# Kernel optimization log

Measured on AMD Instinct MI355X. Metric: run time of the kernel, lower is better.

## Reference

```python
import jax, jax.numpy as jnp
import numpy as np

N_NODES = 40000
N_EDGES = 640000
D_IN = 128
D_HID = 128
D_OUT = 128
N_GRAPHS = 128


def setup_inputs() -> dict:
    key = jax.random.key(0)
    ks = jax.random.split(key, 12)
    x = jax.random.normal(ks[0], (N_NODES, D_IN), dtype=jnp.float32)
    edge_index = jax.random.randint(ks[1], (2, N_EDGES), 0, N_NODES, dtype=jnp.int64)
    batch = jnp.sort(jax.random.randint(ks[2], (N_NODES,), 0, N_GRAPHS, dtype=jnp.int64))
    def lin(k, fan_in, shape):
        s = 1.0 / np.sqrt(fan_in)
        return jax.random.uniform(k, shape, dtype=jnp.float32, minval=-s, maxval=s)
    return {
        "x": x, "edge_index": edge_index, "batch": batch,
        "W_rel0": lin(ks[3], D_IN, (D_IN, D_HID)), "b_rel0": lin(ks[4], D_IN, (D_HID,)), "W_root0": lin(ks[5], D_IN, (D_IN, D_HID)),
        "W_rel1": lin(ks[6], D_HID, (D_HID, D_HID)), "b_rel1": lin(ks[7], D_HID, (D_HID,)), "W_root1": lin(ks[8], D_HID, (D_HID, D_HID)),
        "W_rel2": lin(ks[9], D_HID, (D_HID, D_OUT)), "b_rel2": lin(ks[10], D_HID, (D_OUT,)), "W_root2": lin(ks[11], D_HID, (D_HID, D_OUT)),
    }


def graph_conv(x, src, dst, W_rel, b_rel, W_root):
    # PyG GraphConv: out_i = Lin_rel(sum_{j in N(i)} x_j) + Lin_root(x_i)
    agg = jax.ops.segment_sum(x[src], dst, num_segments=N_NODES)  # [N, F]
    return agg @ W_rel + b_rel + x @ W_root


def reference(x, edge_index, batch,
              W_rel0, b_rel0, W_root0,
              W_rel1, b_rel1, W_root1,
              W_rel2, b_rel2, W_root2):
    src, dst = edge_index[0], edge_index[1]
    h = graph_conv(x, src, dst, W_rel0, b_rel0, W_root0)
    h = jax.nn.relu(h)  # dropout is identity in eval mode
    h = graph_conv(h, src, dst, W_rel1, b_rel1, W_root1)
    h = jax.nn.relu(h)
    h = graph_conv(h, src, dst, W_rel2, b_rel2, W_root2)
    # global_max_pool over per-node graph ids -> [n_graphs, D_OUT]
    return jax.ops.segment_max(h, batch, num_segments=N_GRAPHS)
```

## Files before the change

### kernel.cpp

```cpp
#include <hip/hip_runtime.h>
#include <hip/hip_bf16.h>
#include <math.h>

#define N_NODES 40000
#define N_EDGES 640000
#define D 128
#define N_GRAPHS 128
#define SCAN_NBLK ((N_NODES + 255) / 256)
#define LDS_STRIDE 68

typedef __attribute__((ext_vector_type(8))) short bf16x8;
typedef __attribute__((ext_vector_type(4))) float f32x4;
typedef __attribute__((ext_vector_type(4))) unsigned int u32x4;

static __device__ __forceinline__ unsigned short f2b(float f) {
    unsigned int u = __float_as_uint(f);
    unsigned int r = (u + 0x7fffu + ((u >> 16) & 1u)) >> 16;
    return (unsigned short)r;
}
static __device__ __forceinline__ float blo(unsigned int u) {
    return __uint_as_float(u << 16);
}
static __device__ __forceinline__ float bhi(unsigned int u) {
    return __uint_as_float(u & 0xffff0000u);
}

__global__ void k_hist(const int* __restrict__ ei, int* __restrict__ counts) {
    int e = blockIdx.x * blockDim.x + threadIdx.x;
    if (e < N_EDGES) atomicAdd(&counts[ei[N_EDGES + e]], 1);
}

__global__ void __launch_bounds__(256) k_scan1(const int* __restrict__ counts,
                                               int* __restrict__ local_pre,
                                               int* __restrict__ blocksums) {
    int t = threadIdx.x;
    int i = blockIdx.x * 256 + t;
    int lane = t & 63, wave = t >> 6;
    int v = (i < N_NODES) ? ((counts[i] + 7) & ~7) : 0;
    int incl = v;
#pragma unroll
    for (int off = 1; off < 64; off <<= 1) {
        int u = __shfl_up(incl, off);
        if (lane >= off) incl += u;
    }
    __shared__ int ws[4];
    if (lane == 63) ws[wave] = incl;
    __syncthreads();
    int base = 0;
    for (int w = 0; w < 4; ++w) {
        int s = ws[w];
        if (w < wave) base += s;
    }
    if (i < N_NODES) local_pre[i] = base + incl - v;
    if (t == 255) blocksums[blockIdx.x] = base + incl;
}

__global__ void __launch_bounds__(256) k_scan2(int* __restrict__ blocksums) {
    int t = threadIdx.x;
    int lane = t & 63, wave = t >> 6;
    int v = (t < SCAN_NBLK) ? blocksums[t] : 0;
    int incl = v;
#pragma unroll
    for (int off = 1; off < 64; off <<= 1) {
        int u = __shfl_up(incl, off);
        if (lane >= off) incl += u;
    }
    __shared__ int ws[4];
    if (lane == 63) ws[wave] = incl;
    __syncthreads();
    int base = 0;
    for (int w = 0; w < 4; ++w) {
        int s = ws[w];
        if (w < wave) base += s;
    }
    if (t < SCAN_NBLK) blocksums[t] = base + incl - v;
}

__global__ void __launch_bounds__(256) k_scan3(const int* __restrict__ local_pre,
                                               const int* __restrict__ blocksums,
                                               const int* __restrict__ counts,
                                               int* __restrict__ rp_pad,
                                               int* __restrict__ cursor) {
    int i = blockIdx.x * 256 + threadIdx.x;
    if (i < N_NODES) {
        int rp = blocksums[blockIdx.x] + local_pre[i];
        rp_pad[i] = rp;
        cursor[i] = rp;
        if (i == N_NODES - 1) rp_pad[N_NODES] = rp + ((counts[i] + 7) & ~7);
    }
}

__global__ void k_scatter(const int* __restrict__ ei, int* __restrict__ cursor,
                          int* __restrict__ src_pad) {
    int e = blockIdx.x * blockDim.x + threadIdx.x;
    if (e < N_EDGES) {
        int d = ei[N_EDGES + e];
        int pos = atomicAdd(&cursor[d], 1);
        src_pad[pos] = ei[e];
    }
}

__global__ void k_pad(const int* __restrict__ cursor, const int* __restrict__ rp_pad,
                      int* __restrict__ src_pad) {
    int i = blockIdx.x * blockDim.x + threadIdx.x;
    if (i >= N_NODES) return;
    int s = cursor[i], e = rp_pad[i + 1];
    for (int j = s; j < e; ++j) src_pad[j] = N_NODES;
}

__global__ void k_bounds(const int* __restrict__ batch, int* __restrict__ bounds) {
    int n = blockIdx.x * blockDim.x + threadIdx.x;
    if (n >= N_NODES) return;
    int b = batch[n];
    if (n == 0) {
        for (int g = 0; g <= b; ++g) bounds[g] = 0;
    } else {
        int pb = batch[n - 1];
        for (int g = pb + 1; g <= b; ++g) bounds[g] = n;
    }
    if (n == N_NODES - 1) {
        for (int g = b + 1; g <= N_GRAPHS; ++g) bounds[g] = N_NODES;
    }
}

__global__ void k_x2b(const float* __restrict__ x, unsigned int* __restrict__ xb) {
    int i = blockIdx.x * blockDim.x + threadIdx.x;
    if (i >= N_NODES * D / 8) return;
    const f32x4* xv = (const f32x4*)x;
    f32x4 v0 = xv[i * 2], v1 = xv[i * 2 + 1];
    u32x4 o;
    o.x = ((unsigned int)f2b(v0.y) << 16) | f2b(v0.x);
    o.y = ((unsigned int)f2b(v0.w) << 16) | f2b(v0.z);
    o.z = ((unsigned int)f2b(v1.y) << 16) | f2b(v1.x);
    o.w = ((unsigned int)f2b(v1.w) << 16) | f2b(v1.z);
    ((u32x4*)xb)[i] = o;
}

__global__ void k_wprep3(const float* __restrict__ Wr0, const float* __restrict__ Wt0,
                         const float* __restrict__ Wr1, const float* __restrict__ Wt1,
                         const float* __restrict__ Wr2, const float* __restrict__ Wt2,
                         unsigned short* __restrict__ WT) {
    int l = blockIdx.x >> 7, c = blockIdx.x & 127, k = threadIdx.x;
    const float* Wrel = (l == 0) ? Wr0 : (l == 1) ? Wr1 : Wr2;
    const float* Wroot = (l == 0) ? Wt0 : (l == 1) ? Wt1 : Wt2;
    float v = (k < D) ? Wrel[k * D + c] : Wroot[(k - D) * D + c];
    WT[(size_t)l * 128 * 256 + c * 256 + k] = f2b(v);
}

__global__ void __launch_bounds__(256) k_layer(
    const unsigned short* __restrict__ in,
    const int* __restrict__ rp_pad,
    const int* __restrict__ src_pad,
    const unsigned short* __restrict__ WT,
    const float* __restrict__ bias,
    unsigned short* __restrict__ out,
    int relu) {
    __shared__ unsigned int aggLDS[16 * LDS_STRIDE];
    int tid = threadIdx.x;
    int w = tid >> 6;
    int lane = tid & 63;
    int q = lane >> 4;
    int c = lane & 15;
    int nl = w * 4 + q;
    int nodebase = blockIdx.x * 16;
    const u32x4* inv = (const u32x4*)in;

    int s = rp_pad[nodebase + nl];
    int e = rp_pad[nodebase + nl + 1];
    const int4* sidx = (const int4*)(src_pad + s);
    int ntrips = (e - s) >> 3;

    float a0 = 0.f, a1 = 0.f, a2 = 0.f, a3 = 0.f;
    float a4 = 0.f, a5 = 0.f, a6 = 0.f, a7 = 0.f;

#define ACC8(v) do { \
        a0 += blo((v).x); a1 += bhi((v).x); \
        a2 += blo((v).y); a3 += bhi((v).y); \
        a4 += blo((v).z); a5 += bhi((v).z); \
        a6 += blo((v).w); a7 += bhi((v).w); } while (0)

    for (int t = 0; t < ntrips; ++t) {
        int4 ia = sidx[2 * t];
        int4 ib = sidx[2 * t + 1];
        u32x4 v0 = inv[ia.x * 16 + c];
        u32x4 v1 = inv[ia.y * 16 + c];
        u32x4 v2 = inv[ia.z * 16 + c];
        u32x4 v3 = inv[ia.w * 16 + c];
        u32x4 v4 = inv[ib.x * 16 + c];
        u32x4 v5 = inv[ib.y * 16 + c];
        u32x4 v6 = inv[ib.z * 16 + c];
        u32x4 v7 = inv[ib.w * 16 + c];
        ACC8(v0); ACC8(v1); ACC8(v2); ACC8(v3);
        ACC8(v4); ACC8(v5); ACC8(v6); ACC8(v7);
    }
#undef ACC8

    u32x4 o;
    o.x = ((unsigned int)f2b(a1) << 16) | f2b(a0);
    o.y = ((unsigned int)f2b(a3) << 16) | f2b(a2);
    o.z = ((unsigned int)f2b(a5) << 16) | f2b(a4);
    o.w = ((unsigned int)f2b(a7) << 16) | f2b(a6);
    *(u32x4*)&aggLDS[nl * LDS_STRIDE + c * 4] = o;
    __syncthreads();

    int row = c, quad = q;
    int colbase = w * 32;

    f32x4 acc0 = {0.f, 0.f, 0.f, 0.f};
    f32x4 acc1 = {0.f, 0.f, 0.f, 0.f};

    const unsigned int* Al = &aggLDS[row * LDS_STRIDE];
    const short* Xp = (const short*)(in + (nodebase + row) * D);
    const short* W0 = (const short*)(WT + (colbase + row) * 256);
    const short* W1 = (const short*)(WT + (colbase + 16 + row) * 256);

#pragma unroll
    for (int t = 0; t < 4; ++t) {
        bf16x8 af = *(const bf16x8*)(Al + t * 16 + quad * 4);
        int k0 = t * 32 + quad * 8;
        bf16x8 b0 = *(const bf16x8*)(W0 + k0);
        bf16x8 b1 = *(const bf16x8*)(W1 + k0);
        acc0 = __builtin_amdgcn_mfma_f32_16x16x32_bf16(af, b0, acc0, 0, 0, 0);
        acc1 = __builtin_amdgcn_mfma_f32_16x16x32_bf16(af, b1, acc1, 0, 0, 0);
    }
#pragma unroll
    for (int t = 0; t < 4; ++t) {
        int k0 = t * 32 + quad * 8;
        bf16x8 xf = *(const bf16x8*)(Xp + k0);
        bf16x8 b0 = *(const bf16x8*)(W0 + 128 + k0);
        bf16x8 b1 = *(const bf16x8*)(W1 + 128 + k0);
        acc0 = __builtin_amdgcn_mfma_f32_16x16x32_bf16(xf, b0, acc0, 0, 0, 0);
        acc1 = __builtin_amdgcn_mfma_f32_16x16x32_bf16(xf, b1, acc1, 0, 0, 0);
    }

    int c0 = colbase + row, c1 = c0 + 16;
    float bia0 = bias[c0], bia1 = bias[c1];
#pragma unroll
    for (int r = 0; r < 4; ++r) {
        int n2 = nodebase + quad * 4 + r;
        float v0 = acc0[r] + bia0;
        float v1 = acc1[r] + bia1;
        if (relu) { v0 = fmaxf(v0, 0.f); v1 = fmaxf(v1, 0.f); }
        out[n2 * D + c0] = f2b(v0);
        out[n2 * D + c1] = f2b(v1);
    }
}

__global__ void __launch_bounds__(512) k_segmax(const unsigned short* __restrict__ h,
                                                const int* __restrict__ bounds,
                                                float* __restrict__ out) {
    __shared__ float sm[8][128];
    int g = blockIdx.x;
    int tid = threadIdx.x;
    int rg = tid >> 6;
    int c = tid & 63;
    int s = bounds[g], e = bounds[g + 1];
    const unsigned int* h32 = (const unsigned int*)h;

    float m0 = -INFINITY, m1 = -INFINITY;
    int n = s + rg;
    for (; n + 8 < e; n += 16) {
        unsigned int v0 = h32[n * 64 + c];
        unsigned int v1 = h32[(n + 8) * 64 + c];
        m0 = fmaxf(m0, blo(v0)); m1 = fmaxf(m1, bhi(v0));
        m0 = fmaxf(m0, blo(v1)); m1 = fmaxf(m1, bhi(v1));
    }
    if (n < e) {
        unsigned int v0 = h32[n * 64 + c];
        m0 = fmaxf(m0, blo(v0)); m1 = fmaxf(m1, bhi(v0));
    }
    sm[rg][c * 2] = m0;
    sm[rg][c * 2 + 1] = m1;
    __syncthreads();
    if (tid < 128) {
        float m = sm[0][tid];
#pragma unroll
        for (int r = 1; r < 8; ++r) m = fmaxf(m, sm[r][tid]);
        out[g * D + tid] = m;
    }
}

extern "C" void kernel_launch(void* const* d_in, const int* in_sizes, int n_in,
                              void* d_out, int out_size, void* d_ws, size_t ws_size,
                              hipStream_t stream) {
    const float* x = (const float*)d_in[0];
    const int* ei = (const int*)d_in[1];
    const int* batch = (const int*)d_in[2];
    const float* Wrel[3]  = {(const float*)d_in[3], (const float*)d_in[6], (const float*)d_in[9]};
    const float* brel[3]  = {(const float*)d_in[4], (const float*)d_in[7], (const float*)d_in[10]};
    const float* Wroot[3] = {(const float*)d_in[5], (const float*)d_in[8], (const float*)d_in[11]};
    float* out = (float*)d_out;

    char* ws = (char*)d_ws;
    size_t off = 0;
    auto alloc = [&](size_t bytes) -> void* {
        void* p = ws + off;
        off = (off + bytes + 255) & ~(size_t)255;
        return p;
    };
    unsigned short* xb  = (unsigned short*)alloc((size_t)(N_NODES + 1) * D * 2);
    unsigned short* hA  = (unsigned short*)alloc((size_t)(N_NODES + 1) * D * 2);
    unsigned short* hB  = (unsigned short*)alloc((size_t)(N_NODES + 1) * D * 2);
    unsigned short* WT  = (unsigned short*)alloc((size_t)3 * 128 * 256 * 2);
    int* rp_pad     = (int*)alloc((size_t)(N_NODES + 1) * 4);
    int* counts     = (int*)alloc((size_t)N_NODES * 4);
    int* cursor     = (int*)alloc((size_t)N_NODES * 4);
    int* src_pad    = (int*)alloc((size_t)(N_EDGES + 8 * N_NODES) * 4);
    int* bounds     = (int*)alloc((size_t)(N_GRAPHS + 1) * 4);
    int* local_pre  = (int*)alloc((size_t)N_NODES * 4);
    int* blocksums  = (int*)alloc((size_t)SCAN_NBLK * 4);

    hipMemsetAsync(counts, 0, (size_t)N_NODES * 4, stream);
    hipMemsetAsync(xb + (size_t)N_NODES * D, 0, D * 2, stream);
    hipMemsetAsync(hA + (size_t)N_NODES * D, 0, D * 2, stream);
    hipMemsetAsync(hB + (size_t)N_NODES * D, 0, D * 2, stream);

    k_hist<<<(N_EDGES + 255) / 256, 256, 0, stream>>>(ei, counts);
    k_scan1<<<SCAN_NBLK, 256, 0, stream>>>(counts, local_pre, blocksums);
    k_scan2<<<1, 256, 0, stream>>>(blocksums);
    k_scan3<<<SCAN_NBLK, 256, 0, stream>>>(local_pre, blocksums, counts, rp_pad, cursor);
    k_scatter<<<(N_EDGES + 255) / 256, 256, 0, stream>>>(ei, cursor, src_pad);
    k_pad<<<SCAN_NBLK, 256, 0, stream>>>(cursor, rp_pad, src_pad);
    k_bounds<<<(N_NODES + 255) / 256, 256, 0, stream>>>(batch, bounds);

    k_x2b<<<(N_NODES * D / 8 + 255) / 256, 256, 0, stream>>>(x, (unsigned int*)xb);
    k_wprep3<<<384, 256, 0, stream>>>(Wrel[0], Wroot[0], Wrel[1], Wroot[1],
                                      Wrel[2], Wroot[2], WT);

    const unsigned short* in = xb;
    unsigned short* houts[3] = {hA, hB, hA};
    for (int l = 0; l < 3; ++l) {
        k_layer<<<N_NODES / 16, 256, 0, stream>>>(in, rp_pad, src_pad,
                                                  WT + (size_t)l * 128 * 256,
                                                  brel[l], houts[l], (l < 2) ? 1 : 0);
        in = houts[l];
    }

    k_segmax<<<N_GRAPHS, 512, 0, stream>>>(houts[2], bounds, out);
}
```

Measured before the change: 295.6 us.

## Fuse preprocessing kernels and pad neighbor lists to multiples of sixteen

Four memsets and several small preprocessing kernels (histogram, bounds, x-to-bf16 conversion, weight packing, padding) are merged into two launches, k_init and k_pack1, and padding is moved into the scan step. Each node's neighbor list is now padded to a multiple of 16 instead of 8, so the aggregation loop issues 16 independent gathers per iteration. The aim is to cut launch overhead and raise memory-level parallelism in the gather. In exchange, padding gathers of the zero row grow, since each node now averages about 16 edges against a padded length of up to 31.

```diff
diff --git a/kernel.cpp b/kernel.cpp
--- a/kernel.cpp
+++ b/kernel.cpp
@@ -25,9 +25,66 @@
     return __uint_as_float(u & 0xffff0000u);
 }
 
-__global__ void k_hist(const int* __restrict__ ei, int* __restrict__ counts) {
-    int e = blockIdx.x * blockDim.x + threadIdx.x;
-    if (e < N_EDGES) atomicAdd(&counts[ei[N_EDGES + e]], 1);
+__global__ void __launch_bounds__(256) k_init(
+    const int* __restrict__ batch, int* __restrict__ counts,
+    int* __restrict__ bounds,
+    unsigned short* __restrict__ xb, unsigned short* __restrict__ hA,
+    unsigned short* __restrict__ hB) {
+    int n = blockIdx.x * 256 + threadIdx.x;
+    if (n < N_NODES) {
+        counts[n] = 0;
+        int b = batch[n];
+        if (n == 0) {
+            for (int g = 0; g <= b; ++g) bounds[g] = 0;
+        } else {
+            int pb = batch[n - 1];
+            for (int g = pb + 1; g <= b; ++g) bounds[g] = n;
+        }
+        if (n == N_NODES - 1) {
+            for (int g = b + 1; g <= N_GRAPHS; ++g) bounds[g] = N_NODES;
+        }
+    }
+    if (blockIdx.x == SCAN_NBLK) {
+        int t = threadIdx.x;
+        if (t < 48) {
+            int row = t >> 4, c = t & 15;
+            unsigned short* p = (row == 0) ? xb : (row == 1) ? hA : hB;
+            u32x4 z = {0u, 0u, 0u, 0u};
+            ((u32x4*)(p + (size_t)N_NODES * D))[c] = z;
+        }
+    }
+}
+
+__global__ void __launch_bounds__(256) k_pack1(
+    const int* __restrict__ ei, int* __restrict__ counts,
+    const float* __restrict__ x, unsigned int* __restrict__ xb,
+    const float* __restrict__ Wr0, const float* __restrict__ Wt0,
+    const float* __restrict__ Wr1, const float* __restrict__ Wt1,
+    const float* __restrict__ Wr2, const float* __restrict__ Wt2,
+    unsigned short* __restrict__ WT) {
+    int b = blockIdx.x;
+    int t = threadIdx.x;
+    if (b < 2500) {
+        int e = b * 256 + t;
+        atomicAdd(&counts[ei[N_EDGES + e]], 1);
+    } else if (b < 5000) {
+        int i = (b - 2500) * 256 + t;
+        const f32x4* xv = (const f32x4*)x;
+        f32x4 v0 = xv[i * 2], v1 = xv[i * 2 + 1];
+        u32x4 o;
+        o.x = ((unsigned int)f2b(v0.y) << 16) | f2b(v0.x);
+        o.y = ((unsigned int)f2b(v0.w) << 16) | f2b(v0.z);
+        o.z = ((unsigned int)f2b(v1.y) << 16) | f2b(v1.x);
+        o.w = ((unsigned int)f2b(v1.w) << 16) | f2b(v1.z);
+        ((u32x4*)xb)[i] = o;
+    } else {
+        int bw = b - 5000;
+        int l = bw >> 7, c = bw & 127, k = t;
+        const float* Wrel = (l == 0) ? Wr0 : (l == 1) ? Wr1 : Wr2;
+        const float* Wroot = (l == 0) ? Wt0 : (l == 1) ? Wt1 : Wt2;
+        float v = (k < D) ? Wrel[k * D + c] : Wroot[(k - D) * D + c];
+        WT[(size_t)l * 128 * 256 + c * 256 + k] = f2b(v);
+    }
 }
 
 __global__ void __launch_bounds__(256) k_scan1(const int* __restrict__ counts,
@@ -36,7 +93,7 @@
     int t = threadIdx.x;
     int i = blockIdx.x * 256 + t;
     int lane = t & 63, wave = t >> 6;
-    int v = (i < N_NODES) ? ((counts[i] + 7) & ~7) : 0;
+    int v = (i < N_NODES) ? ((counts[i] + 15) & ~15) : 0;
     int incl = v;
 #pragma unroll
     for (int off = 1; off < 64; off <<= 1) {
@@ -80,13 +137,17 @@
                                                const int* __restrict__ blocksums,
                                                const int* __restrict__ counts,
                                                int* __restrict__ rp_pad,
-                                               int* __restrict__ cursor) {
+                                               int* __restrict__ cursor,
+                                               int* __restrict__ src_pad) {
     int i = blockIdx.x * 256 + threadIdx.x;
     if (i < N_NODES) {
         int rp = blocksums[blockIdx.x] + local_pre[i];
         rp_pad[i] = rp;
         cursor[i] = rp;
-        if (i == N_NODES - 1) rp_pad[N_NODES] = rp + ((counts[i] + 7) & ~7);
+        int c = counts[i];
+        int pc = (c + 15) & ~15;
+        for (int j = rp + c; j < rp + pc; ++j) src_pad[j] = N_NODES;
+        if (i == N_NODES - 1) rp_pad[N_NODES] = rp + pc;
     }
 }
 
@@ -98,53 +159,6 @@
         int pos = atomicAdd(&cursor[d], 1);
         src_pad[pos] = ei[e];
     }
-}
-
-__global__ void k_pad(const int* __restrict__ cursor, const int* __restrict__ rp_pad,
-                      int* __restrict__ src_pad) {
-    int i = blockIdx.x * blockDim.x + threadIdx.x;
-    if (i >= N_NODES) return;
-    int s = cursor[i], e = rp_pad[i + 1];
-    for (int j = s; j < e; ++j) src_pad[j] = N_NODES;
-}
-
-__global__ void k_bounds(const int* __restrict__ batch, int* __restrict__ bounds) {
-    int n = blockIdx.x * blockDim.x + threadIdx.x;
-    if (n >= N_NODES) return;
-    int b = batch[n];
-    if (n == 0) {
-        for (int g = 0; g <= b; ++g) bounds[g] = 0;
-    } else {
-        int pb = batch[n - 1];
-        for (int g = pb + 1; g <= b; ++g) bounds[g] = n;
-    }
-    if (n == N_NODES - 1) {
-        for (int g = b + 1; g <= N_GRAPHS; ++g) bounds[g] = N_NODES;
-    }
-}
-
-__global__ void k_x2b(const float* __restrict__ x, unsigned int* __restrict__ xb) {
-    int i = blockIdx.x * blockDim.x + threadIdx.x;
-    if (i >= N_NODES * D / 8) return;
-    const f32x4* xv = (const f32x4*)x;
-    f32x4 v0 = xv[i * 2], v1 = xv[i * 2 + 1];
-    u32x4 o;
-    o.x = ((unsigned int)f2b(v0.y) << 16) | f2b(v0.x);
-    o.y = ((unsigned int)f2b(v0.w) << 16) | f2b(v0.z);
-    o.z = ((unsigned int)f2b(v1.y) << 16) | f2b(v1.x);
-    o.w = ((unsigned int)f2b(v1.w) << 16) | f2b(v1.z);
-    ((u32x4*)xb)[i] = o;
-}
-
-__global__ void k_wprep3(const float* __restrict__ Wr0, const float* __restrict__ Wt0,
-                         const float* __restrict__ Wr1, const float* __restrict__ Wt1,
-                         const float* __restrict__ Wr2, const float* __restrict__ Wt2,
-                         unsigned short* __restrict__ WT) {
-    int l = blockIdx.x >> 7, c = blockIdx.x & 127, k = threadIdx.x;
-    const float* Wrel = (l == 0) ? Wr0 : (l == 1) ? Wr1 : Wr2;
-    const float* Wroot = (l == 0) ? Wt0 : (l == 1) ? Wt1 : Wt2;
-    float v = (k < D) ? Wrel[k * D + c] : Wroot[(k - D) * D + c];
-    WT[(size_t)l * 128 * 256 + c * 256 + k] = f2b(v);
 }
 
 __global__ void __launch_bounds__(256) k_layer(
@@ -168,7 +182,7 @@
     int s = rp_pad[nodebase + nl];
     int e = rp_pad[nodebase + nl + 1];
     const int4* sidx = (const int4*)(src_pad + s);
-    int ntrips = (e - s) >> 3;
+    int ntrips = (e - s) >> 4;
 
     float a0 = 0.f, a1 = 0.f, a2 = 0.f, a3 = 0.f;
     float a4 = 0.f, a5 = 0.f, a6 = 0.f, a7 = 0.f;
@@ -180,8 +194,10 @@
         a6 += blo((v).w); a7 += bhi((v).w); } while (0)
 
     for (int t = 0; t < ntrips; ++t) {
-        int4 ia = sidx[2 * t];
-        int4 ib = sidx[2 * t + 1];
+        int4 ia = sidx[4 * t + 0];
+        int4 ib = sidx[4 * t + 1];
+        int4 ic = sidx[4 * t + 2];
+        int4 id = sidx[4 * t + 3];
         u32x4 v0 = inv[ia.x * 16 + c];
         u32x4 v1 = inv[ia.y * 16 + c];
         u32x4 v2 = inv[ia.z * 16 + c];
@@ -190,8 +206,18 @@
         u32x4 v5 = inv[ib.y * 16 + c];
         u32x4 v6 = inv[ib.z * 16 + c];
         u32x4 v7 = inv[ib.w * 16 + c];
+        u32x4 v8 = inv[ic.x * 16 + c];
+        u32x4 v9 = inv[ic.y * 16 + c];
+        u32x4 va = inv[ic.z * 16 + c];
+        u32x4 vb = inv[ic.w * 16 + c];
+        u32x4 vc = inv[id.x * 16 + c];
+        u32x4 vd = inv[id.y * 16 + c];
+        u32x4 ve = inv[id.z * 16 + c];
+        u32x4 vf = inv[id.w * 16 + c];
         ACC8(v0); ACC8(v1); ACC8(v2); ACC8(v3);
         ACC8(v4); ACC8(v5); ACC8(v6); ACC8(v7);
+        ACC8(v8); ACC8(v9); ACC8(va); ACC8(vb);
+        ACC8(vc); ACC8(vd); ACC8(ve); ACC8(vf);
     }
 #undef ACC8
 
@@ -305,27 +331,20 @@
     int* rp_pad     = (int*)alloc((size_t)(N_NODES + 1) * 4);
     int* counts     = (int*)alloc((size_t)N_NODES * 4);
     int* cursor     = (int*)alloc((size_t)N_NODES * 4);
-    int* src_pad    = (int*)alloc((size_t)(N_EDGES + 8 * N_NODES) * 4);
+    int* src_pad    = (int*)alloc((size_t)(N_EDGES + 16 * N_NODES) * 4);
     int* bounds     = (int*)alloc((size_t)(N_GRAPHS + 1) * 4);
     int* local_pre  = (int*)alloc((size_t)N_NODES * 4);
     int* blocksums  = (int*)alloc((size_t)SCAN_NBLK * 4);
 
-    hipMemsetAsync(counts, 0, (size_t)N_NODES * 4, stream);
-    hipMemsetAsync(xb + (size_t)N_NODES * D, 0, D * 2, stream);
-    hipMemsetAsync(hA + (size_t)N_NODES * D, 0, D * 2, stream);
-    hipMemsetAsync(hB + (size_t)N_NODES * D, 0, D * 2, stream);
-
-    k_hist<<<(N_EDGES + 255) / 256, 256, 0, stream>>>(ei, counts);
+    k_init<<<SCAN_NBLK + 1, 256, 0, stream>>>(batch, counts, bounds, xb, hA, hB);
+    k_pack1<<<5384, 256, 0, stream>>>(ei, counts, x, (unsigned int*)xb,
+                                      Wrel[0], Wroot[0], Wrel[1], Wroot[1],
+                                      Wrel[2], Wroot[2], WT);
     k_scan1<<<SCAN_NBLK, 256, 0, stream>>>(counts, local_pre, blocksums);
     k_scan2<<<1, 256, 0, stream>>>(blocksums);
-    k_scan3<<<SCAN_NBLK, 256, 0, stream>>>(local_pre, blocksums, counts, rp_pad, cursor);
+    k_scan3<<<SCAN_NBLK, 256, 0, stream>>>(local_pre, blocksums, counts,
+                                           rp_pad, cursor, src_pad);
     k_scatter<<<(N_EDGES + 255) / 256, 256, 0, stream>>>(ei, cursor, src_pad);
-    k_pad<<<SCAN_NBLK, 256, 0, stream>>>(cursor, rp_pad, src_pad);
-    k_bounds<<<(N_NODES + 255) / 256, 256, 0, stream>>>(batch, bounds);
-
-    k_x2b<<<(N_NODES * D / 8 + 255) / 256, 256, 0, stream>>>(x, (unsigned int*)xb);
-    k_wprep3<<<384, 256, 0, stream>>>(Wrel[0], Wroot[0], Wrel[1], Wroot[1],
-                                      Wrel[2], Wroot[2], WT);
 
     const unsigned short* in = xb;
     unsigned short* houts[3] = {hA, hB, hA};
```

Result: faster. 281.6 us (-4.7%).
